# Kernel optimization log

Measured on AMD Instinct MI355X. Metric: run time of the kernel, lower is better.

The kernel has to match this reference:

```python
import jax, jax.numpy as jnp
import numpy as np

N, LQ, C, M, L, P = 8, 2048, 256, 8, 4, 4
DH = C // M  # 32
LENS = (2048, 1024, 512, 256)


def setup_inputs() -> dict:
    key = jax.random.key(0)
    ks = jax.random.split(key, 8)
    s = 1.0 / np.sqrt(C)
    return {
        "query": jax.random.normal(ks[0], (N, LQ, C), jnp.float32),
        "reference_points": jax.random.uniform(ks[1], (N, LQ, L, 1), jnp.float32),
        "input_flatten": jax.random.normal(ks[2], (N, sum(LENS), C), jnp.float32),
        "temporal_lens": np.array(LENS, np.int64),
        "level_start_index": np.array([0, 2048, 3072, 3584], np.int64),
        "W_off": jax.random.normal(ks[3], (C, M * L * P), jnp.float32) * 0.01,
        "b_off": jax.random.normal(ks[4], (M * L * P,), jnp.float32),
        "W_attn": jax.random.normal(ks[5], (C, M * L * P), jnp.float32) * 0.01,
        "b_attn": jnp.zeros((M * L * P,), jnp.float32),
        "W_val": jax.random.normal(ks[6], (C, C), jnp.float32) * s,
        "b_val": jnp.zeros((C,), jnp.float32),
        "W_out": jax.random.normal(ks[7], (C, C), jnp.float32) * s,
        "b_out": jnp.zeros((C,), jnp.float32),
    }


def _deform_core(value, lens, loc, attn):
    # value: (N, S, M, DH); loc, attn: (N, LQ, M, L, P); loc in normalized [0,1] coords.
    # Equivalent to per-level F.grid_sample (bilinear, zeros padding, align_corners=False)
    # on a 1xT image: pixel position = loc*T - 0.5; the y-coord 0.5 lands exactly on row 0.
    outs = []
    start = 0
    for l, T in enumerate(lens):
        v = value[:, start:start + T].transpose(0, 2, 1, 3)  # (N, M, T, DH)
        start += T
        pos = loc[..., l, :] * T - 0.5                       # (N, LQ, M, P)
        x0f = jnp.floor(pos)
        frac = pos - x0f
        x0 = x0f.astype(jnp.int32)

        def gather(idx):
            i = jnp.clip(idx, 0, T - 1).transpose(0, 2, 1, 3).reshape(N, M, LQ * P, 1)
            return jnp.take_along_axis(v, i, axis=2).reshape(N, M, LQ, P, DH)

        in0 = ((x0 >= 0) & (x0 < T)).astype(value.dtype)
        in1 = ((x0 + 1 >= 0) & (x0 + 1 < T)).astype(value.dtype)
        w0 = ((1.0 - frac) * in0).transpose(0, 2, 1, 3)[..., None]  # (N, M, LQ, P, 1)
        w1 = (frac * in1).transpose(0, 2, 1, 3)[..., None]
        outs.append(gather(x0) * w0 + gather(x0 + 1) * w1)          # (N, M, LQ, P, DH)
    sampled = jnp.stack(outs, axis=3)          # (N, M, LQ, L, P, DH)
    aw = attn.transpose(0, 2, 1, 3, 4)         # (N, M, LQ, L, P)
    return jnp.einsum('nmqlpd,nmqlp->nqmd', sampled, aw).reshape(N, LQ, C)


def reference(query, reference_points, input_flatten, temporal_lens, level_start_index,
              W_off, b_off, W_attn, b_attn, W_val, b_val, W_out, b_out):
    lens = [int(t) for t in np.asarray(temporal_lens)[:L]]  # static per-level lengths
    value = (input_flatten @ W_val + b_val).reshape(N, -1, M, DH)
    off = (query @ W_off + b_off).reshape(N, LQ, M, L, P)
    attn = jax.nn.softmax((query @ W_attn + b_attn).reshape(N, LQ, M, L * P), axis=-1)
    attn = attn.reshape(N, LQ, M, L, P)
    norm = jnp.asarray(lens, query.dtype)                    # offset_normalizer (L,)
    loc = reference_points[:, :, None, :, None, 0] + off / norm[None, None, None, :, None]
    out = _deform_core(value, lens, loc, attn)
    out = out @ W_out + b_out
    return out, loc, attn
```

## Files before the change

### kernel.cpp

```cpp
#include <hip/hip_runtime.h>
#include <hip/hip_bf16.h>
#include <math.h>

#define NB 8
#define LQ 2048
#define SSUM 3840

typedef unsigned short ushort_t;
typedef unsigned int uint_t;
typedef __attribute__((ext_vector_type(8))) short bf16x8;
typedef __attribute__((ext_vector_type(4))) float f32x4;

__device__ __forceinline__ ushort_t f2bf(float f) {
  __hip_bfloat16 h = __float2bfloat16(f);
  return *reinterpret_cast<ushort_t*>(&h);
}
__device__ __forceinline__ uint_t pk2bf(float lo, float hi) {
  float2 t; t.x = lo; t.y = hi;
  __hip_bfloat162 h = __float22bfloat162_rn(t);
  return *reinterpret_cast<uint_t*>(&h);
}
__device__ __forceinline__ float bf2f_lo(uint_t u) {
  union { uint_t u32; float f; } x;
  x.u32 = u << 16;
  return x.f;
}
__device__ __forceinline__ float bf2f_hi(uint_t u) {
  union { uint_t u32; float f; } x;
  x.u32 = u & 0xffff0000u;
  return x.f;
}
__device__ __forceinline__ void ld_lds16(const void* g, void* l) {
  __builtin_amdgcn_global_load_lds(
      (const __attribute__((address_space(1))) void*)g,
      (__attribute__((address_space(3))) void*)l, 16, 0, 0);
}

__global__ __launch_bounds__(256) void prep(
    const float* __restrict__ W_val, const float* __restrict__ W_off,
    const float* __restrict__ W_attn, const float* __restrict__ W_out,
    ushort_t* __restrict__ BtVal, ushort_t* __restrict__ BtOA,
    ushort_t* __restrict__ BtOut) {
  const int b = blockIdx.x, t = threadIdx.x;
  if (b < 256) { BtVal[b * 256 + t] = f2bf(W_val[(size_t)t * 256 + b]); return; }
  if (b < 512) { int n = b - 256; BtOut[n * 256 + t] = f2bf(W_out[(size_t)t * 256 + n]); return; }
  if (b < 640) { int n = b - 512; BtOA[n * 256 + t] = f2bf(W_off[(size_t)t * 128 + n]); return; }
  int n = b - 640; BtOA[(128 + n) * 256 + t] = f2bf(W_attn[(size_t)t * 128 + n]);
}

template <bool AF32>
__global__ __launch_bounds__(256) void gemm_fused(
    int job_base,
    const float* __restrict__ in_flat, const float* __restrict__ query,
    const ushort_t* __restrict__ core,
    const ushort_t* __restrict__ BtVal, const ushort_t* __restrict__ BtOA,
    const ushort_t* __restrict__ BtOut,
    const float* __restrict__ b_val, const float* __restrict__ b_off,
    const float* __restrict__ b_attn, const float* __restrict__ b_out,
    ushort_t* __restrict__ value, float* __restrict__ loc,
    float* __restrict__ attn, float* __restrict__ out) {
  __shared__ ushort_t Ab[2][64][32];
  __shared__ ushort_t Bb[2][256][32];

  const int job = job_base + blockIdx.x;

  const float* Afp = nullptr;
  const ushort_t* Abf = nullptr;
  const ushort_t* Bt;
  const float* bias_lo; const float* bias_hi;
  int bm, cstride;
  ushort_t* Cb = nullptr;
  float* Cf_lo = nullptr; float* Cf_hi = nullptr;

  if (job < 480) {
    bm = job * 64; Afp = in_flat; Bt = BtVal;
    bias_lo = b_val; bias_hi = b_val + 128; Cb = value; cstride = 256;
  } else if (job < 736) {
    bm = (job - 480) * 64; Afp = query; Bt = BtOA;
    bias_lo = b_off; bias_hi = b_attn; Cf_lo = loc; Cf_hi = attn; cstride = 128;
  } else {
    bm = (job - 736) * 64; Abf = core; Bt = BtOut;
    bias_lo = b_out; bias_hi = b_out + 128; Cf_lo = out; Cf_hi = out + 128;
    cstride = 256;
  }

  const int tid = threadIdx.x;
  const int lane = tid & 63;
  const int wv = tid >> 6;
  const int quad = lane >> 4;
  const int l16 = lane & 15;
  const int wm = (wv >> 1) * 32;
  const int wn = (wv & 1) * 128;
  const int drow = lane >> 2;
  const int dk = (lane & 3) * 8;

  const int asr = tid >> 2;
  const int ask = (tid & 3) * 8;

  f32x4 acc[2][8];
#pragma unroll
  for (int i = 0; i < 2; ++i)
#pragma unroll
    for (int j = 0; j < 8; ++j) acc[i][j] = (f32x4)(0.f);

  auto stageB = [&](int db, int k0) {
#pragma unroll
    for (int c = 0; c < 4; ++c)
      ld_lds16(Bt + (size_t)(wv * 64 + c * 16 + drow) * 256 + k0 + dk,
               &Bb[db][wv * 64 + c * 16 + drow][dk]);
  };
  auto stageA_dma = [&](int db, int k0) {
    ld_lds16(Abf + (size_t)(bm + wv * 16 + drow) * 256 + k0 + dk,
             &Ab[db][wv * 16 + drow][dk]);
  };
  auto stageA_f32 = [&](int db, int k0) {
    const float* gp = Afp + (size_t)(bm + asr) * 256 + k0 + ask;
    float4 f0 = *(const float4*)gp;
    float4 f1 = *(const float4*)(gp + 4);
    uint4 c;
    c.x = pk2bf(f0.x, f0.y);
    c.y = pk2bf(f0.z, f0.w);
    c.z = pk2bf(f1.x, f1.y);
    c.w = pk2bf(f1.z, f1.w);
    *(uint4*)&Ab[db][asr][ask] = c;
  };

  if (AF32) stageA_f32(0, 0); else stageA_dma(0, 0);
  stageB(0, 0);

#pragma unroll
  for (int it = 0; it < 8; ++it) {
    const int db = it & 1;
    __syncthreads();
    if (it < 7) {
      if (AF32) stageA_f32(db ^ 1, (it + 1) * 32); else stageA_dma(db ^ 1, (it + 1) * 32);
      stageB(db ^ 1, (it + 1) * 32);
    }
    bf16x8 af[2], bfr[8];
#pragma unroll
    for (int mi = 0; mi < 2; ++mi)
      af[mi] = *(const bf16x8*)&Ab[db][wm + mi * 16 + l16][quad * 8];
#pragma unroll
    for (int ni = 0; ni < 8; ++ni)
      bfr[ni] = *(const bf16x8*)&Bb[db][wn + ni * 16 + l16][quad * 8];
#pragma unroll
    for (int mi = 0; mi < 2; ++mi)
#pragma unroll
      for (int ni = 0; ni < 8; ++ni)
        acc[mi][ni] = __builtin_amdgcn_mfma_f32_16x16x32_bf16(af[mi], bfr[ni], acc[mi][ni], 0, 0, 0);
  }

  const int hi = wv & 1;
  const float* bias = hi ? bias_hi : bias_lo;
  ushort_t* Cbw = Cb ? (Cb + (hi ? 128 : 0)) : nullptr;
  float* Cfw = hi ? Cf_hi : Cf_lo;

#pragma unroll
  for (int ni = 0; ni < 8; ++ni) {
    int cc = ni * 16 + l16;
    float bv = bias[cc];
#pragma unroll
    for (int mi = 0; mi < 2; ++mi) {
      f32x4 v = acc[mi][ni];
      int rbase = bm + wm + mi * 16 + quad * 4;
#pragma unroll
      for (int r = 0; r < 4; ++r) {
        float o = v[r] + bv;
        size_t idx = (size_t)(rbase + r) * cstride + cc;
        if (Cbw) Cbw[idx] = f2bf(o);
        else     Cfw[idx] = o;
      }
    }
  }
}

__global__ __launch_bounds__(256) void deform_fused(
    const ushort_t* __restrict__ value,
    float* __restrict__ locbuf,
    float* __restrict__ attnbuf,
    const float* __restrict__ refp,
    ushort_t* __restrict__ core) {
  const int tid = threadIdx.x;
  const int nq0 = blockIdx.x * 4;
  const int n = nq0 >> 11;

  __shared__ float slv[512];
  __shared__ float slog[512];
  __shared__ float4 sp[512];

  const float rnorm[4] = {1.f / 2048.f, 1.f / 1024.f, 1.f / 512.f, 1.f / 256.f};
  const int lensA[4] = {2048, 1024, 512, 256};
  const int startsA[4] = {0, 2048, 3072, 3584};

#pragma unroll
  for (int j = 0; j < 2; ++j) {
    int s = tid + j * 256;
    int q = s >> 7;
    int r = s & 127;
    int l = (r >> 2) & 3;
    float lv = refp[(size_t)(nq0 + q) * 4 + l] +
               locbuf[(size_t)nq0 * 128 + s] * rnorm[l];
    locbuf[(size_t)nq0 * 128 + s] = lv;
    slv[s] = lv;
    slog[s] = attnbuf[(size_t)nq0 * 128 + s];
  }
  __syncthreads();

  if (tid < 32) {
    int base = tid * 16;
    float v[16];
#pragma unroll
    for (int i = 0; i < 16; ++i) v[i] = slog[base + i];
    float mx = v[0];
#pragma unroll
    for (int i = 1; i < 16; ++i) mx = fmaxf(mx, v[i]);
    float ssum = 0.f;
#pragma unroll
    for (int i = 0; i < 16; ++i) { v[i] = __expf(v[i] - mx); ssum += v[i]; }
    float rs = 1.f / ssum;
    float* gout = attnbuf + (size_t)nq0 * 128 + base;
#pragma unroll
    for (int i = 0; i < 16; ++i) {
      float pv = v[i] * rs;
      slog[base + i] = pv;
      gout[i] = pv;
    }
  }
  __syncthreads();

#pragma unroll
  for (int j = 0; j < 2; ++j) {
    int s = tid + j * 256;
    int q = s >> 7;
    int r = s & 127;
    int m = r >> 4;
    int lp = r & 15;
    int l = lp >> 2;
    int T = lensA[l];
    float lv = slv[s];
    float aw = slog[s];
    float pos = lv * (float)T - 0.5f;
    float x0f = floorf(pos);
    float fr = pos - x0f;
    int x0 = (int)x0f;
    float w0 = ((unsigned)x0 < (unsigned)T) ? (1.f - fr) * aw : 0.f;
    float w1 = ((unsigned)(x0 + 1) < (unsigned)T) ? fr * aw : 0.f;
    int i0 = min(max(x0, 0), T - 1);
    int i1 = min(max(x0 + 1, 0), T - 1);
    float4 pr;
    pr.x = w0;
    pr.y = w1;
    pr.z = __int_as_float((startsA[l] + i0) * 256);
    pr.w = __int_as_float((startsA[l] + i1) * 256);
    sp[q * 128 + lp * 8 + m] = pr;
  }
  __syncthreads();

  const int q = tid >> 6;
  const int t64 = tid & 63;
  const int m = t64 >> 3;
  const int g = t64 & 7;
  const ushort_t* vbase = value + (size_t)n * (SSUM * 256) + m * 32 + g * 4;

  float a0 = 0.f, a1 = 0.f, a2 = 0.f, a3 = 0.f;
#pragma unroll
  for (int lp = 0; lp < 16; ++lp) {
    float4 pr = sp[q * 128 + lp * 8 + m];
    int o0 = __float_as_int(pr.z);
    int o1 = __float_as_int(pr.w);
    uint2 u0 = *(const uint2*)(vbase + o0);
    uint2 u1 = *(const uint2*)(vbase + o1);
    a0 += pr.x * bf2f_lo(u0.x) + pr.y * bf2f_lo(u1.x);
    a1 += pr.x * bf2f_hi(u0.x) + pr.y * bf2f_hi(u1.x);
    a2 += pr.x * bf2f_lo(u0.y) + pr.y * bf2f_lo(u1.y);
    a3 += pr.x * bf2f_hi(u0.y) + pr.y * bf2f_hi(u1.y);
  }
  uint2 outp;
  outp.x = (uint_t)f2bf(a0) | ((uint_t)f2bf(a1) << 16);
  outp.y = (uint_t)f2bf(a2) | ((uint_t)f2bf(a3) << 16);
  *(uint2*)&core[(size_t)(nq0 + q) * 256 + m * 32 + g * 4] = outp;
}

extern "C" void kernel_launch(void* const* d_in, const int* in_sizes, int n_in,
                              void* d_out, int out_size, void* d_ws, size_t ws_size,
                              hipStream_t stream) {
  const float* query    = (const float*)d_in[0];
  const float* refpts   = (const float*)d_in[1];
  const float* in_flat  = (const float*)d_in[2];
  const float* W_off  = (const float*)d_in[5];
  const float* b_off  = (const float*)d_in[6];
  const float* W_attn = (const float*)d_in[7];
  const float* b_attn = (const float*)d_in[8];
  const float* W_val  = (const float*)d_in[9];
  const float* b_val  = (const float*)d_in[10];
  const float* W_out  = (const float*)d_in[11];
  const float* b_out  = (const float*)d_in[12];

  float* out  = (float*)d_out;
  float* loc  = out + (size_t)NB * LQ * 256;
  float* attn = loc + (size_t)NB * LQ * 128;

  ushort_t* value = (ushort_t*)d_ws;
  ushort_t* core  = value + (size_t)NB * SSUM * 256;
  ushort_t* BtVal = core + (size_t)NB * LQ * 256;
  ushort_t* BtOA  = BtVal + 65536;
  ushort_t* BtOut = BtOA + 65536;

  const int Mq = NB * LQ;

  prep<<<768, 256, 0, stream>>>(W_val, W_off, W_attn, W_out, BtVal, BtOA, BtOut);

  gemm_fused<true><<<736, 256, 0, stream>>>(
      0, in_flat, query, core, BtVal, BtOA, BtOut,
      b_val, b_off, b_attn, b_out, value, loc, attn, out);

  deform_fused<<<Mq / 4, 256, 0, stream>>>(value, loc, attn, refpts, core);

  gemm_fused<false><<<256, 256, 0, stream>>>(
      736, in_flat, query, core, BtVal, BtOA, BtOut,
      b_val, b_off, b_attn, b_out, value, loc, attn, out);
}
```

Baseline: 164.2 us.

## Fuse output projection GEMM into deformable sampling kernel via LDS core tile

The deformable sampling kernel now handles 16 queries per block. It keeps the sampled core tile (16x256 bf16) in shared memory and runs the output projection MFMA directly, so the separate output GEMM launch and the global round trip of the core buffer are gone. Location, softmax and sampling-parameter setup are merged into one per-(query, head) thread pass with vectorised loads. In exchange, the B operand (BtOut) is read straight from global memory for every block without LDS staging, and the 16-row M tile gives poor MFMA efficiency.

```diff
diff --git a/kernel.cpp b/kernel.cpp
--- a/kernel.cpp
+++ b/kernel.cpp
@@ -48,24 +48,19 @@
   int n = b - 640; BtOA[(128 + n) * 256 + t] = f2bf(W_attn[(size_t)t * 128 + n]);
 }
 
-template <bool AF32>
 __global__ __launch_bounds__(256) void gemm_fused(
-    int job_base,
     const float* __restrict__ in_flat, const float* __restrict__ query,
-    const ushort_t* __restrict__ core,
     const ushort_t* __restrict__ BtVal, const ushort_t* __restrict__ BtOA,
-    const ushort_t* __restrict__ BtOut,
     const float* __restrict__ b_val, const float* __restrict__ b_off,
-    const float* __restrict__ b_attn, const float* __restrict__ b_out,
+    const float* __restrict__ b_attn,
     ushort_t* __restrict__ value, float* __restrict__ loc,
-    float* __restrict__ attn, float* __restrict__ out) {
+    float* __restrict__ attn) {
   __shared__ ushort_t Ab[2][64][32];
   __shared__ ushort_t Bb[2][256][32];
 
-  const int job = job_base + blockIdx.x;
-
-  const float* Afp = nullptr;
-  const ushort_t* Abf = nullptr;
+  const int job = blockIdx.x;
+
+  const float* Afp;
   const ushort_t* Bt;
   const float* bias_lo; const float* bias_hi;
   int bm, cstride;
@@ -75,13 +70,9 @@
   if (job < 480) {
     bm = job * 64; Afp = in_flat; Bt = BtVal;
     bias_lo = b_val; bias_hi = b_val + 128; Cb = value; cstride = 256;
-  } else if (job < 736) {
+  } else {
     bm = (job - 480) * 64; Afp = query; Bt = BtOA;
     bias_lo = b_off; bias_hi = b_attn; Cf_lo = loc; Cf_hi = attn; cstride = 128;
-  } else {
-    bm = (job - 736) * 64; Abf = core; Bt = BtOut;
-    bias_lo = b_out; bias_hi = b_out + 128; Cf_lo = out; Cf_hi = out + 128;
-    cstride = 256;
   }
 
   const int tid = threadIdx.x;
@@ -90,10 +81,8 @@
   const int quad = lane >> 4;
   const int l16 = lane & 15;
   const int wm = (wv >> 1) * 32;
-  const int wn = (wv & 1) * 128;
   const int drow = lane >> 2;
   const int dk = (lane & 3) * 8;
-
   const int asr = tid >> 2;
   const int ask = (tid & 3) * 8;
 
@@ -109,11 +98,7 @@
       ld_lds16(Bt + (size_t)(wv * 64 + c * 16 + drow) * 256 + k0 + dk,
                &Bb[db][wv * 64 + c * 16 + drow][dk]);
   };
-  auto stageA_dma = [&](int db, int k0) {
-    ld_lds16(Abf + (size_t)(bm + wv * 16 + drow) * 256 + k0 + dk,
-             &Ab[db][wv * 16 + drow][dk]);
-  };
-  auto stageA_f32 = [&](int db, int k0) {
+  auto stageA = [&](int db, int k0) {
     const float* gp = Afp + (size_t)(bm + asr) * 256 + k0 + ask;
     float4 f0 = *(const float4*)gp;
     float4 f1 = *(const float4*)(gp + 4);
@@ -125,7 +110,7 @@
     *(uint4*)&Ab[db][asr][ask] = c;
   };
 
-  if (AF32) stageA_f32(0, 0); else stageA_dma(0, 0);
+  stageA(0, 0);
   stageB(0, 0);
 
 #pragma unroll
@@ -133,7 +118,7 @@
     const int db = it & 1;
     __syncthreads();
     if (it < 7) {
-      if (AF32) stageA_f32(db ^ 1, (it + 1) * 32); else stageA_dma(db ^ 1, (it + 1) * 32);
+      stageA(db ^ 1, (it + 1) * 32);
       stageB(db ^ 1, (it + 1) * 32);
     }
     bf16x8 af[2], bfr[8];
@@ -142,7 +127,7 @@
       af[mi] = *(const bf16x8*)&Ab[db][wm + mi * 16 + l16][quad * 8];
 #pragma unroll
     for (int ni = 0; ni < 8; ++ni)
-      bfr[ni] = *(const bf16x8*)&Bb[db][wn + ni * 16 + l16][quad * 8];
+      bfr[ni] = *(const bf16x8*)&Bb[db][(wv & 1) * 128 + ni * 16 + l16][quad * 8];
 #pragma unroll
     for (int mi = 0; mi < 2; ++mi)
 #pragma unroll
@@ -174,111 +159,146 @@
   }
 }
 
-__global__ __launch_bounds__(256) void deform_fused(
+__global__ __launch_bounds__(256) void deform_out(
     const ushort_t* __restrict__ value,
     float* __restrict__ locbuf,
     float* __restrict__ attnbuf,
     const float* __restrict__ refp,
-    ushort_t* __restrict__ core) {
+    const ushort_t* __restrict__ BtOut,
+    const float* __restrict__ b_out,
+    float* __restrict__ out) {
   const int tid = threadIdx.x;
-  const int nq0 = blockIdx.x * 4;
+  const int nq0 = blockIdx.x * 16;
   const int n = nq0 >> 11;
 
-  __shared__ float slv[512];
-  __shared__ float slog[512];
-  __shared__ float4 sp[512];
+  __shared__ float4 sp[2048];
+  __shared__ ushort_t coreT[16 * 264];
 
   const float rnorm[4] = {1.f / 2048.f, 1.f / 1024.f, 1.f / 512.f, 1.f / 256.f};
   const int lensA[4] = {2048, 1024, 512, 256};
   const int startsA[4] = {0, 2048, 3072, 3584};
 
-#pragma unroll
-  for (int j = 0; j < 2; ++j) {
-    int s = tid + j * 256;
-    int q = s >> 7;
-    int r = s & 127;
-    int l = (r >> 2) & 3;
-    float lv = refp[(size_t)(nq0 + q) * 4 + l] +
-               locbuf[(size_t)nq0 * 128 + s] * rnorm[l];
-    locbuf[(size_t)nq0 * 128 + s] = lv;
-    slv[s] = lv;
-    slog[s] = attnbuf[(size_t)nq0 * 128 + s];
+  if (tid < 128) {
+    const int q = tid >> 3, m = tid & 7;
+    const size_t base = (size_t)(nq0 + q) * 128 + m * 16;
+    float lv[16], lg[16];
+#pragma unroll
+    for (int i = 0; i < 4; ++i) {
+      float4 a = *(const float4*)&locbuf[base + i * 4];
+      float4 b = *(const float4*)&attnbuf[base + i * 4];
+      lv[i * 4 + 0] = a.x; lv[i * 4 + 1] = a.y; lv[i * 4 + 2] = a.z; lv[i * 4 + 3] = a.w;
+      lg[i * 4 + 0] = b.x; lg[i * 4 + 1] = b.y; lg[i * 4 + 2] = b.z; lg[i * 4 + 3] = b.w;
+    }
+    float4 rp = *(const float4*)&refp[(size_t)(nq0 + q) * 4];
+    const float rpv[4] = {rp.x, rp.y, rp.z, rp.w};
+#pragma unroll
+    for (int lp = 0; lp < 16; ++lp) {
+      int l = lp >> 2;
+      lv[lp] = rpv[l] + lv[lp] * rnorm[l];
+    }
+#pragma unroll
+    for (int i = 0; i < 4; ++i) {
+      float4 a;
+      a.x = lv[i * 4 + 0]; a.y = lv[i * 4 + 1]; a.z = lv[i * 4 + 2]; a.w = lv[i * 4 + 3];
+      *(float4*)&locbuf[base + i * 4] = a;
+    }
+    float mx = lg[0];
+#pragma unroll
+    for (int i = 1; i < 16; ++i) mx = fmaxf(mx, lg[i]);
+    float ssum = 0.f;
+#pragma unroll
+    for (int i = 0; i < 16; ++i) { lg[i] = __expf(lg[i] - mx); ssum += lg[i]; }
+    float rs = 1.f / ssum;
+#pragma unroll
+    for (int i = 0; i < 16; ++i) lg[i] *= rs;
+#pragma unroll
+    for (int i = 0; i < 4; ++i) {
+      float4 a;
+      a.x = lg[i * 4 + 0]; a.y = lg[i * 4 + 1]; a.z = lg[i * 4 + 2]; a.w = lg[i * 4 + 3];
+      *(float4*)&attnbuf[base + i * 4] = a;
+    }
+#pragma unroll
+    for (int lp = 0; lp < 16; ++lp) {
+      int l = lp >> 2;
+      int T = lensA[l];
+      float pos = lv[lp] * (float)T - 0.5f;
+      float x0f = floorf(pos);
+      float fr = pos - x0f;
+      int x0 = (int)x0f;
+      float aw = lg[lp];
+      float w0 = ((unsigned)x0 < (unsigned)T) ? (1.f - fr) * aw : 0.f;
+      float w1 = ((unsigned)(x0 + 1) < (unsigned)T) ? fr * aw : 0.f;
+      int i0 = min(max(x0, 0), T - 1);
+      int i1 = min(max(x0 + 1, 0), T - 1);
+      float4 pr;
+      pr.x = w0;
+      pr.y = w1;
+      pr.z = __int_as_float((startsA[l] + i0) * 256);
+      pr.w = __int_as_float((startsA[l] + i1) * 256);
+      sp[q * 128 + lp * 8 + m] = pr;
+    }
   }
   __syncthreads();
 
-  if (tid < 32) {
-    int base = tid * 16;
-    float v[16];
-#pragma unroll
-    for (int i = 0; i < 16; ++i) v[i] = slog[base + i];
-    float mx = v[0];
-#pragma unroll
-    for (int i = 1; i < 16; ++i) mx = fmaxf(mx, v[i]);
-    float ssum = 0.f;
-#pragma unroll
-    for (int i = 0; i < 16; ++i) { v[i] = __expf(v[i] - mx); ssum += v[i]; }
-    float rs = 1.f / ssum;
-    float* gout = attnbuf + (size_t)nq0 * 128 + base;
-#pragma unroll
-    for (int i = 0; i < 16; ++i) {
-      float pv = v[i] * rs;
-      slog[base + i] = pv;
-      gout[i] = pv;
-    }
+#pragma unroll
+  for (int j = 0; j < 4; ++j) {
+    int task = j * 256 + tid;
+    int q = task >> 6;
+    int m = (task >> 3) & 7;
+    int g = task & 7;
+    const ushort_t* vbase = value + (size_t)n * (SSUM * 256) + m * 32 + g * 4;
+    float a0 = 0.f, a1 = 0.f, a2 = 0.f, a3 = 0.f;
+#pragma unroll
+    for (int lp = 0; lp < 16; ++lp) {
+      float4 pr = sp[q * 128 + lp * 8 + m];
+      int o0 = __float_as_int(pr.z);
+      int o1 = __float_as_int(pr.w);
+      uint2 u0 = *(const uint2*)(vbase + o0);
+      uint2 u1 = *(const uint2*)(vbase + o1);
+      a0 += pr.x * bf2f_lo(u0.x) + pr.y * bf2f_lo(u1.x);
+      a1 += pr.x * bf2f_hi(u0.x) + pr.y * bf2f_hi(u1.x);
+      a2 += pr.x * bf2f_lo(u0.y) + pr.y * bf2f_lo(u1.y);
+      a3 += pr.x * bf2f_hi(u0.y) + pr.y * bf2f_hi(u1.y);
+    }
+    uint2 cp;
+    cp.x = (uint_t)f2bf(a0) | ((uint_t)f2bf(a1) << 16);
+    cp.y = (uint_t)f2bf(a2) | ((uint_t)f2bf(a3) << 16);
+    *(uint2*)&coreT[q * 264 + m * 32 + g * 4] = cp;
   }
   __syncthreads();
 
-#pragma unroll
-  for (int j = 0; j < 2; ++j) {
-    int s = tid + j * 256;
-    int q = s >> 7;
-    int r = s & 127;
-    int m = r >> 4;
-    int lp = r & 15;
-    int l = lp >> 2;
-    int T = lensA[l];
-    float lv = slv[s];
-    float aw = slog[s];
-    float pos = lv * (float)T - 0.5f;
-    float x0f = floorf(pos);
-    float fr = pos - x0f;
-    int x0 = (int)x0f;
-    float w0 = ((unsigned)x0 < (unsigned)T) ? (1.f - fr) * aw : 0.f;
-    float w1 = ((unsigned)(x0 + 1) < (unsigned)T) ? fr * aw : 0.f;
-    int i0 = min(max(x0, 0), T - 1);
-    int i1 = min(max(x0 + 1, 0), T - 1);
-    float4 pr;
-    pr.x = w0;
-    pr.y = w1;
-    pr.z = __int_as_float((startsA[l] + i0) * 256);
-    pr.w = __int_as_float((startsA[l] + i1) * 256);
-    sp[q * 128 + lp * 8 + m] = pr;
-  }
-  __syncthreads();
-
-  const int q = tid >> 6;
-  const int t64 = tid & 63;
-  const int m = t64 >> 3;
-  const int g = t64 & 7;
-  const ushort_t* vbase = value + (size_t)n * (SSUM * 256) + m * 32 + g * 4;
-
-  float a0 = 0.f, a1 = 0.f, a2 = 0.f, a3 = 0.f;
-#pragma unroll
-  for (int lp = 0; lp < 16; ++lp) {
-    float4 pr = sp[q * 128 + lp * 8 + m];
-    int o0 = __float_as_int(pr.z);
-    int o1 = __float_as_int(pr.w);
-    uint2 u0 = *(const uint2*)(vbase + o0);
-    uint2 u1 = *(const uint2*)(vbase + o1);
-    a0 += pr.x * bf2f_lo(u0.x) + pr.y * bf2f_lo(u1.x);
-    a1 += pr.x * bf2f_hi(u0.x) + pr.y * bf2f_hi(u1.x);
-    a2 += pr.x * bf2f_lo(u0.y) + pr.y * bf2f_lo(u1.y);
-    a3 += pr.x * bf2f_hi(u0.y) + pr.y * bf2f_hi(u1.y);
-  }
-  uint2 outp;
-  outp.x = (uint_t)f2bf(a0) | ((uint_t)f2bf(a1) << 16);
-  outp.y = (uint_t)f2bf(a2) | ((uint_t)f2bf(a3) << 16);
-  *(uint2*)&core[(size_t)(nq0 + q) * 256 + m * 32 + g * 4] = outp;
+  const int lane = tid & 63;
+  const int wv = tid >> 6;
+  const int quad = lane >> 4;
+  const int l16 = lane & 15;
+  const int wn = wv * 64;
+
+  f32x4 acc[4];
+#pragma unroll
+  for (int i = 0; i < 4; ++i) acc[i] = (f32x4)(0.f);
+
+#pragma unroll
+  for (int kk = 0; kk < 8; ++kk) {
+    const int k0 = kk * 32;
+    bf16x8 af = *(const bf16x8*)&coreT[l16 * 264 + k0 + quad * 8];
+#pragma unroll
+    for (int ni = 0; ni < 4; ++ni) {
+      bf16x8 bfr = *(const bf16x8*)(BtOut + (size_t)(wn + ni * 16 + l16) * 256 + k0 + quad * 8);
+      acc[ni] = __builtin_amdgcn_mfma_f32_16x16x32_bf16(af, bfr, acc[ni], 0, 0, 0);
+    }
+  }
+
+#pragma unroll
+  for (int ni = 0; ni < 4; ++ni) {
+    int col = wn + ni * 16 + l16;
+    float bv = b_out[col];
+    f32x4 v = acc[ni];
+#pragma unroll
+    for (int r = 0; r < 4; ++r) {
+      int q = quad * 4 + r;
+      out[(size_t)(nq0 + q) * 256 + col] = v[r] + bv;
+    }
+  }
 }
 
 extern "C" void kernel_launch(void* const* d_in, const int* in_sizes, int n_in,
@@ -301,8 +321,7 @@
   float* attn = loc + (size_t)NB * LQ * 128;
 
   ushort_t* value = (ushort_t*)d_ws;
-  ushort_t* core  = value + (size_t)NB * SSUM * 256;
-  ushort_t* BtVal = core + (size_t)NB * LQ * 256;
+  ushort_t* BtVal = value + (size_t)NB * SSUM * 256;
   ushort_t* BtOA  = BtVal + 65536;
   ushort_t* BtOut = BtOA + 65536;
 
@@ -310,13 +329,9 @@
 
   prep<<<768, 256, 0, stream>>>(W_val, W_off, W_attn, W_out, BtVal, BtOA, BtOut);
 
-  gemm_fused<true><<<736, 256, 0, stream>>>(
-      0, in_flat, query, core, BtVal, BtOA, BtOut,
-      b_val, b_off, b_attn, b_out, value, loc, attn, out);
-
-  deform_fused<<<Mq / 4, 256, 0, stream>>>(value, loc, attn, refpts, core);
-
-  gemm_fused<false><<<256, 256, 0, stream>>>(
-      736, in_flat, query, core, BtVal, BtOA, BtOut,
-      b_val, b_off, b_attn, b_out, value, loc, attn, out);
-}
+  gemm_fused<<<736, 256, 0, stream>>>(
+      in_flat, query, BtVal, BtOA, b_val, b_off, b_attn, value, loc, attn);
+
+  deform_out<<<Mq / 16, 256, 0, stream>>>(
+      value, loc, attn, refpts, BtOut, b_out, out);
+}
```

Measured after the change: 168.9 us. 2.9% more time.
